# Kernel optimization log

Hardware: AMD Instinct MI355X
Metric: run time of the kernel (lower is better)

The kernel has to match this reference:

```python
import jax, jax.numpy as jnp
import numpy as np

CLAMP = 60.0
EPS = 1e-4

def _make_weights(N, alpha_logits, delta_logits, beta_logits):
    alpha = jax.nn.sigmoid(alpha_logits)   # [C,H]
    delta = jax.nn.sigmoid(delta_logits)
    beta = jax.nn.sigmoid(beta_logits)
    A = alpha * beta                        # [C,H]
    r = jnp.clip(1.0 - alpha * delta, EPS, 1.0 - EPS)
    t = jnp.arange(N, dtype=jnp.float32)[:, None, None]   # [N,1,1]
    logr = jnp.clip(jnp.log(r) * t, -CLAMP, CLAMP)        # [N,C,H]
    return A, jnp.exp(logr), jnp.exp(-logr)

def _ema_fwd(x, A, eta, r_pos, r_neg):
    # x: [B,N,C] -> y: [B,N,C]
    z = A * x[..., None] * r_neg            # [B,N,C,H]
    h = jnp.cumsum(z, axis=1) * r_pos       # [B,N,C,H]
    return jnp.sum(eta * h, axis=-1)        # [B,N,C]

def reference(x, alpha_logits, delta_logits, beta_logits, eta, proj_w, proj_b):
    B, N, C = x.shape
    A, r_pos, r_neg = _make_weights(N, alpha_logits, delta_logits, beta_logits)
    xf = x.astype(jnp.float32)
    y_fwd = _ema_fwd(xf, A, eta, r_pos, r_neg)
    y_bwd = _ema_fwd(xf[:, ::-1], A, eta, r_pos, r_neg)[:, ::-1]
    z = jnp.concatenate([y_fwd, y_bwd], axis=-1).astype(x.dtype)  # [B,N,2C]
    return z @ proj_w.T + proj_b            # [B,N,C]

def setup_inputs():
    key = jax.random.key(0)
    ks = jax.random.split(key, 7)
    B, N, C, H = 8, 4096, 512, 4
    return {
        "x": jax.random.normal(ks[0], (B, N, C), dtype=jnp.float32),
        "alpha_logits": jax.random.normal(ks[1], (C, H), dtype=jnp.float32),
        "delta_logits": jax.random.normal(ks[2], (C, H), dtype=jnp.float32),
        "beta_logits": jax.random.normal(ks[3], (C, H), dtype=jnp.float32),
        "eta": jax.random.normal(ks[4], (C, H), dtype=jnp.float32) * 0.02,
        "proj_w": jax.random.normal(ks[5], (C, 2 * C), dtype=jnp.float32) / np.sqrt(2.0 * C),
        "proj_b": jax.random.normal(ks[6], (C,), dtype=jnp.float32) * 0.01,
    }
```

## Files before the change

kernel.cpp:

```cpp
#include <hip/hip_runtime.h>
#include <hip/hip_bf16.h>

#define B_ 8
#define N_ 4096
#define C_ 512
#define H_ 4
#define EPS_ 1e-4f
#define E60P 1.14200739e26f
#define E60M 8.7565108e-27f

typedef __attribute__((ext_vector_type(8))) short short8;
typedef __attribute__((ext_vector_type(4))) float floatx4;
typedef unsigned short ushort_t;

__device__ __forceinline__ float sigmoidf_(float v) {
    return 1.0f / (1.0f + expf(-v));
}

__device__ __forceinline__ int pk_off(int t, int w, int k0, int ks, int f,
                                      int lane8, int kb) {
    return ((((t * 2 + w) * 16 + k0) * 2 + ks) * 4 + f) * 512 + lane8 * 8 + kb;
}

__global__ __launch_bounds__(256) void k_partials3(
    const float* __restrict__ x, const float* __restrict__ al,
    const float* __restrict__ dl, const float* __restrict__ bl,
    float* __restrict__ P)
{
    int bid   = blockIdx.x;
    int chunk = bid & 15;
    int ct    = (bid >> 4) & 7;
    int b     = bid >> 7;
    int lane  = threadIdx.x & 63;
    int wave  = threadIdx.x >> 6;
    int c     = ct * 64 + lane;
    int sub   = chunk * 4 + wave;
    int t0f   = sub * 64;
    int t0b   = (63 - sub) * 64;

    float aa[4], dd[4], bb[4];
    { float4 v = ((const float4*)al)[c]; aa[0]=v.x; aa[1]=v.y; aa[2]=v.z; aa[3]=v.w; }
    { float4 v = ((const float4*)dl)[c]; dd[0]=v.x; dd[1]=v.y; dd[2]=v.z; dd[3]=v.w; }
    { float4 v = ((const float4*)bl)[c]; bb[0]=v.x; bb[1]=v.y; bb[2]=v.z; bb[3]=v.w; }

    float A[H_], ri[H_], Lh[H_];
    #pragma unroll
    for (int h = 0; h < H_; ++h) {
        float alpha = sigmoidf_(aa[h]);
        float delta = sigmoidf_(dd[h]);
        float beta  = sigmoidf_(bb[h]);
        A[h] = alpha * beta;
        float r = fminf(fmaxf(1.0f - alpha * delta, EPS_), 1.0f - EPS_);
        Lh[h] = logf(r);
        ri[h] = 1.0f / r;
    }

    const float* xp = x + ((size_t)b * N_ + t0f) * C_ + c;

    float ep[H_], T[H_];
    #pragma unroll
    for (int h = 0; h < H_; ++h) {
        ep[h] = expf(fminf(-Lh[h] * (float)t0f, 60.0f));
        T[h]  = 0.0f;
    }
    #pragma unroll 8
    for (int i = 0; i < 64; ++i) {
        float xv = xp[(size_t)i * C_];
        #pragma unroll
        for (int h = 0; h < H_; ++h) {
            T[h]  = fmaf(A[h] * xv, ep[h], T[h]);
            ep[h] = fminf(ep[h] * ri[h], E60P);
        }
    }
    {
        float* pp = P + ((size_t)b * 64 + sub) * (H_ * C_) + c;
        #pragma unroll
        for (int h = 0; h < H_; ++h) pp[h * C_] = T[h];
    }

    #pragma unroll
    for (int h = 0; h < H_; ++h) {
        ep[h] = expf(fminf(-Lh[h] * (float)t0b, 60.0f));
        T[h]  = 0.0f;
    }
    #pragma unroll 8
    for (int j = 0; j < 64; ++j) {
        float xv = xp[(size_t)(63 - j) * C_];
        #pragma unroll
        for (int h = 0; h < H_; ++h) {
            T[h]  = fmaf(A[h] * xv, ep[h], T[h]);
            ep[h] = fminf(ep[h] * ri[h], E60P);
        }
    }
    {
        float* pp = P + ((size_t)(8 + b) * 64 + (63 - sub)) * (H_ * C_) + c;
        #pragma unroll
        for (int h = 0; h < H_; ++h) pp[h * C_] = T[h];
    }
}

__global__ __launch_bounds__(256) void k_scan(float* __restrict__ P)
{
    int bid = blockIdx.x;
    int ct  = bid & 7;
    int b   = (bid >> 3) & 7;
    int dir = bid >> 6;
    int cl  = threadIdx.x & 63;
    int h   = threadIdx.x >> 6;
    int c   = ct * 64 + cl;

    float run = 0.0f;
    float* base = P + ((size_t)(dir * 8 + b) * 64) * (H_ * C_) + h * C_ + c;
    for (int s = 0; s < 64; ++s) {
        float v = base[s * (H_ * C_)];
        base[s * (H_ * C_)] = run;
        run += v;
    }
}

__global__ __launch_bounds__(256) void k_apply3(
    const float* __restrict__ x, const float* __restrict__ al,
    const float* __restrict__ dl, const float* __restrict__ bl,
    const float* __restrict__ eta, const float* __restrict__ P,
    ushort_t* __restrict__ Zp)
{
    int bid   = blockIdx.x;
    int chunk = bid & 15;
    int ct    = (bid >> 4) & 7;
    int b     = bid >> 7;
    int lane  = threadIdx.x & 63;
    int wave  = threadIdx.x >> 6;
    int c     = ct * 64 + lane;
    int sub   = chunk * 4 + wave;
    int t0f   = sub * 64;
    int t0b   = (63 - sub) * 64;

    int ksv = lane >> 5, qv = (lane >> 3) & 3, kbv = lane & 7;
    int k0f = ct;
    int k0b = 8 + ct;

    float aa[4], dd[4], bb[4], ee[4];
    { float4 v = ((const float4*)al )[c]; aa[0]=v.x; aa[1]=v.y; aa[2]=v.z; aa[3]=v.w; }
    { float4 v = ((const float4*)dl )[c]; dd[0]=v.x; dd[1]=v.y; dd[2]=v.z; dd[3]=v.w; }
    { float4 v = ((const float4*)bl )[c]; bb[0]=v.x; bb[1]=v.y; bb[2]=v.z; bb[3]=v.w; }
    { float4 v = ((const float4*)eta)[c]; ee[0]=v.x; ee[1]=v.y; ee[2]=v.z; ee[3]=v.w; }

    float A[H_], rr[H_], ri[H_], Lh[H_];
    #pragma unroll
    for (int h = 0; h < H_; ++h) {
        float alpha = sigmoidf_(aa[h]);
        float delta = sigmoidf_(dd[h]);
        float beta  = sigmoidf_(bb[h]);
        A[h] = alpha * beta;
        float r = fminf(fmaxf(1.0f - alpha * delta, EPS_), 1.0f - EPS_);
        Lh[h] = logf(r);
        rr[h] = r;
        ri[h] = 1.0f / r;
    }

    const float* xp = x + ((size_t)b * N_ + t0f) * C_ + c;

    {
        const float* cp = P + ((size_t)b * 64 + sub) * (H_ * C_) + c;
        float ep[H_], em[H_], S[H_];
        #pragma unroll
        for (int h = 0; h < H_; ++h) {
            ep[h] = expf(fminf(-Lh[h] * (float)t0f, 60.0f));
            em[h] = expf(fmaxf( Lh[h] * (float)t0f, -60.0f));
            S[h]  = cp[h * C_];
        }
        #pragma unroll 4
        for (int i = 0; i < 64; ++i) {
            int n  = t0f + i;
            float xv = xp[(size_t)i * C_];
            float y = 0.0f;
            #pragma unroll
            for (int h = 0; h < H_; ++h) {
                S[h]  = fmaf(A[h] * xv, ep[h], S[h]);
                ep[h] = fminf(ep[h] * ri[h], E60P);
                y     = fmaf(ee[h], em[h] * S[h], y);
                em[h] = fmaxf(em[h] * rr[h], E60M);
            }
            int rm = n & 127, mt = b * 32 + (n >> 7);
            int off = pk_off(mt, rm >> 6, k0f, ksv, (rm >> 4) & 3,
                             qv * 16 + (rm & 15), kbv);
            __hip_bfloat16 yb = __float2bfloat16(y);
            Zp[off] = *(ushort_t*)&yb;
        }
    }

    {
        const float* cp = P + ((size_t)(8 + b) * 64 + (63 - sub)) * (H_ * C_) + c;
        float ep[H_], em[H_], S[H_];
        #pragma unroll
        for (int h = 0; h < H_; ++h) {
            ep[h] = expf(fminf(-Lh[h] * (float)t0b, 60.0f));
            em[h] = expf(fmaxf( Lh[h] * (float)t0b, -60.0f));
            S[h]  = cp[h * C_];
        }
        #pragma unroll 4
        for (int j = 0; j < 64; ++j) {
            int n  = t0f + 63 - j;
            float xv = xp[(size_t)(63 - j) * C_];
            float y = 0.0f;
            #pragma unroll
            for (int h = 0; h < H_; ++h) {
                S[h]  = fmaf(A[h] * xv, ep[h], S[h]);
                ep[h] = fminf(ep[h] * ri[h], E60P);
                y     = fmaf(ee[h], em[h] * S[h], y);
                em[h] = fmaxf(em[h] * rr[h], E60M);
            }
            int rm = n & 127, mt = b * 32 + (n >> 7);
            int off = pk_off(mt, rm >> 6, k0b, ksv, (rm >> 4) & 3,
                             qv * 16 + (rm & 15), kbv);
            __hip_bfloat16 yb = __float2bfloat16(y);
            Zp[off] = *(ushort_t*)&yb;
        }
    }
}

__global__ __launch_bounds__(256) void k_cvtw2(const float* __restrict__ w,
                                               ushort_t* __restrict__ Wp)
{
    int i = blockIdx.x * 256 + threadIdx.x;
    int n = i >> 10, k = i & 1023;
    int nt = n >> 7, rn = n & 127;
    int k0 = k >> 6, kk = k & 63;
    int off = pk_off(nt, rn >> 6, k0, kk >> 5, (rn >> 4) & 3,
                     ((kk >> 3) & 3) * 16 + (rn & 15), kk & 7);
    __hip_bfloat16 vb = __float2bfloat16(w[i]);
    Wp[off] = *(ushort_t*)&vb;
}

__global__ __launch_bounds__(256, 2) void k_gemm2(
    const ushort_t* __restrict__ Zp, const ushort_t* __restrict__ Wp,
    const float* __restrict__ bias, float* __restrict__ out)
{
    __shared__ __align__(16) float stg[32 * 132];

    int tid  = threadIdx.x;
    int lane = tid & 63, wave = tid >> 6;
    int wm   = wave & 1, wn = wave >> 1;
    int fr   = lane & 15, quad = lane >> 4;

    int lin = blockIdx.x;
    int nt  = lin & 3, mt = lin >> 2;
    int m0  = mt * 128, n0 = nt * 128;

    const ushort_t* Ab = Zp + ((size_t)(mt * 2 + wm) * 16) * 4096 + lane * 8;
    const ushort_t* Bb = Wp + ((size_t)(nt * 2 + wn) * 16) * 4096 + lane * 8;

    floatx4 acc[4][4];
    #pragma unroll
    for (int mf = 0; mf < 4; ++mf)
        #pragma unroll
        for (int nf = 0; nf < 4; ++nf)
            acc[mf][nf] = (floatx4){0.f, 0.f, 0.f, 0.f};

    #pragma unroll
    for (int k0 = 0; k0 < 16; ++k0) {
        short8 af[2][4], bf[2][4];
        #pragma unroll
        for (int ks = 0; ks < 2; ++ks)
            #pragma unroll
            for (int f = 0; f < 4; ++f) {
                af[ks][f] = *(const short8*)(Ab + k0 * 4096 + (ks * 4 + f) * 512);
                bf[ks][f] = *(const short8*)(Bb + k0 * 4096 + (ks * 4 + f) * 512);
            }
        #pragma unroll
        for (int ks = 0; ks < 2; ++ks)
            #pragma unroll
            for (int mf = 0; mf < 4; ++mf)
                #pragma unroll
                for (int nf = 0; nf < 4; ++nf)
                    acc[mf][nf] = __builtin_amdgcn_mfma_f32_16x16x32_bf16(
                        af[ks][mf], bf[ks][nf], acc[mf][nf], 0, 0, 0);
    }

    int rrow = tid >> 3;
    int seg  = tid & 7;
    int gcol = n0 + seg * 16;

    #pragma unroll
    for (int ch = 0; ch < 4; ++ch) {
        if ((wave & 1) == (ch >> 1)) {
            int ml = (ch & 1) * 2;
            #pragma unroll
            for (int mi = 0; mi < 2; ++mi) {
                #pragma unroll
                for (int nf = 0; nf < 4; ++nf) {
                    int col = wn * 64 + nf * 16 + fr;
                    #pragma unroll
                    for (int rg = 0; rg < 4; ++rg) {
                        int row = mi * 16 + quad * 4 + rg;
                        stg[row * 132 + col] = acc[ml + mi][nf][rg];
                    }
                }
            }
        }
        __syncthreads();
        {
            int gm = m0 + ch * 32 + rrow;
            const float* s = &stg[rrow * 132 + seg * 16];
            #pragma unroll
            for (int k = 0; k < 4; ++k) {
                float4 v  = *(const float4*)&s[k * 4];
                float4 bv = *(const float4*)&bias[gcol + k * 4];
                v.x += bv.x; v.y += bv.y; v.z += bv.z; v.w += bv.w;
                *(float4*)&out[(size_t)gm * 512 + gcol + k * 4] = v;
            }
        }
        __syncthreads();
    }
}

extern "C" void kernel_launch(void* const* d_in, const int* in_sizes, int n_in,
                              void* d_out, int out_size, void* d_ws, size_t ws_size,
                              hipStream_t stream)
{
    const float* x  = (const float*)d_in[0];
    const float* al = (const float*)d_in[1];
    const float* dl = (const float*)d_in[2];
    const float* bl = (const float*)d_in[3];
    const float* et = (const float*)d_in[4];
    const float* pw = (const float*)d_in[5];
    const float* pb = (const float*)d_in[6];
    float* out = (float*)d_out;

    ushort_t* Zp = (ushort_t*)d_ws;
    float*    P  = (float*)((char*)d_ws + 67108864);
    ushort_t* Wp = (ushort_t*)((char*)d_ws + 75497472);

    hipLaunchKernelGGL(k_cvtw2,     dim3(2048), dim3(256), 0, stream, pw, Wp);
    hipLaunchKernelGGL(k_partials3, dim3(1024), dim3(256), 0, stream, x, al, dl, bl, P);
    hipLaunchKernelGGL(k_scan,      dim3(128),  dim3(256), 0, stream, P);
    hipLaunchKernelGGL(k_apply3,    dim3(1024), dim3(256), 0, stream, x, al, dl, bl, et, P, Zp);
    hipLaunchKernelGGL(k_gemm2,     dim3(1024), dim3(256), 0, stream, Zp, Wp, pb, out);
}
```

Before: 237.4 us.

## Vectorize EMA scans with packed float2, prefetch x, simplify Zp offsets, remap GEMM blocks

The partials and apply kernels now hold the four decay heads as two float2 vectors so the compiler can emit packed FP32 math, and they load the next 8 timesteps of x while the current 8 are computed. The apply kernel precomputes a base packed-layout offset per thread and adds a cheap per-step term, replacing the full pk_off index calculation. The GEMM block index mapping is changed so consecutive blocks share M tiles across N tiles, aiming at better L2 reuse. The prefetch buffers raise register pressure, and the mixed changes make attribution hard.

```diff
diff --git a/kernel.cpp b/kernel.cpp
--- a/kernel.cpp
+++ b/kernel.cpp
@@ -11,6 +11,7 @@
 
 typedef __attribute__((ext_vector_type(8))) short short8;
 typedef __attribute__((ext_vector_type(4))) float floatx4;
+typedef __attribute__((ext_vector_type(2))) float floatx2;
 typedef unsigned short ushort_t;
 
 __device__ __forceinline__ float sigmoidf_(float v) {
@@ -54,48 +55,85 @@
         Lh[h] = logf(r);
         ri[h] = 1.0f / r;
     }
+    const floatx2 E2P = {E60P, E60P};
+    floatx2 A2[2]  = {{A[0],  A[1]},  {A[2],  A[3]}};
+    floatx2 ri2[2] = {{ri[0], ri[1]}, {ri[2], ri[3]}};
 
     const float* xp = x + ((size_t)b * N_ + t0f) * C_ + c;
 
-    float ep[H_], T[H_];
-    #pragma unroll
-    for (int h = 0; h < H_; ++h) {
-        ep[h] = expf(fminf(-Lh[h] * (float)t0f, 60.0f));
-        T[h]  = 0.0f;
-    }
-    #pragma unroll 8
-    for (int i = 0; i < 64; ++i) {
-        float xv = xp[(size_t)i * C_];
-        #pragma unroll
-        for (int h = 0; h < H_; ++h) {
-            T[h]  = fmaf(A[h] * xv, ep[h], T[h]);
-            ep[h] = fminf(ep[h] * ri[h], E60P);
-        }
+    floatx2 ep2[2], T2[2];
+    #pragma unroll
+    for (int p = 0; p < 2; ++p) {
+        ep2[p] = (floatx2){expf(fminf(-Lh[2*p]   * (float)t0f, 60.0f)),
+                           expf(fminf(-Lh[2*p+1] * (float)t0f, 60.0f))};
+        T2[p]  = (floatx2){0.f, 0.f};
     }
     {
+        float cur[8];
+        #pragma unroll
+        for (int j = 0; j < 8; ++j) cur[j] = xp[(size_t)j * C_];
+        #pragma unroll 1
+        for (int g = 0; g < 8; ++g) {
+            float nxt[8];
+            if (g < 7) {
+                #pragma unroll
+                for (int j = 0; j < 8; ++j)
+                    nxt[j] = xp[(size_t)(g * 8 + 8 + j) * C_];
+            }
+            #pragma unroll
+            for (int j = 0; j < 8; ++j) {
+                floatx2 xv2 = {cur[j], cur[j]};
+                #pragma unroll
+                for (int p = 0; p < 2; ++p) {
+                    T2[p] += (A2[p] * xv2) * ep2[p];
+                    ep2[p] = __builtin_elementwise_min(ep2[p] * ri2[p], E2P);
+                }
+            }
+            if (g < 7) {
+                #pragma unroll
+                for (int j = 0; j < 8; ++j) cur[j] = nxt[j];
+            }
+        }
         float* pp = P + ((size_t)b * 64 + sub) * (H_ * C_) + c;
-        #pragma unroll
-        for (int h = 0; h < H_; ++h) pp[h * C_] = T[h];
-    }
-
-    #pragma unroll
-    for (int h = 0; h < H_; ++h) {
-        ep[h] = expf(fminf(-Lh[h] * (float)t0b, 60.0f));
-        T[h]  = 0.0f;
-    }
-    #pragma unroll 8
-    for (int j = 0; j < 64; ++j) {
-        float xv = xp[(size_t)(63 - j) * C_];
-        #pragma unroll
-        for (int h = 0; h < H_; ++h) {
-            T[h]  = fmaf(A[h] * xv, ep[h], T[h]);
-            ep[h] = fminf(ep[h] * ri[h], E60P);
-        }
+        pp[0]      = T2[0].x;  pp[C_]     = T2[0].y;
+        pp[2 * C_] = T2[1].x;  pp[3 * C_] = T2[1].y;
+    }
+
+    #pragma unroll
+    for (int p = 0; p < 2; ++p) {
+        ep2[p] = (floatx2){expf(fminf(-Lh[2*p]   * (float)t0b, 60.0f)),
+                           expf(fminf(-Lh[2*p+1] * (float)t0b, 60.0f))};
+        T2[p]  = (floatx2){0.f, 0.f};
     }
     {
+        float cur[8];
+        #pragma unroll
+        for (int j = 0; j < 8; ++j) cur[j] = xp[(size_t)(63 - j) * C_];
+        #pragma unroll 1
+        for (int g = 0; g < 8; ++g) {
+            float nxt[8];
+            if (g < 7) {
+                #pragma unroll
+                for (int j = 0; j < 8; ++j)
+                    nxt[j] = xp[(size_t)(63 - (g * 8 + 8 + j)) * C_];
+            }
+            #pragma unroll
+            for (int j = 0; j < 8; ++j) {
+                floatx2 xv2 = {cur[j], cur[j]};
+                #pragma unroll
+                for (int p = 0; p < 2; ++p) {
+                    T2[p] += (A2[p] * xv2) * ep2[p];
+                    ep2[p] = __builtin_elementwise_min(ep2[p] * ri2[p], E2P);
+                }
+            }
+            if (g < 7) {
+                #pragma unroll
+                for (int j = 0; j < 8; ++j) cur[j] = nxt[j];
+            }
+        }
         float* pp = P + ((size_t)(8 + b) * 64 + (63 - sub)) * (H_ * C_) + c;
-        #pragma unroll
-        for (int h = 0; h < H_; ++h) pp[h * C_] = T[h];
+        pp[0]      = T2[0].x;  pp[C_]     = T2[0].y;
+        pp[2 * C_] = T2[1].x;  pp[3 * C_] = T2[1].y;
     }
 }
 
@@ -136,8 +174,10 @@
     int t0b   = (63 - sub) * 64;
 
     int ksv = lane >> 5, qv = (lane >> 3) & 3, kbv = lane & 7;
-    int k0f = ct;
-    int k0b = 8 + ct;
+    int mt  = b * 32 + (t0f >> 7);
+    int wq  = (t0f >> 6) & 1;
+    int offcF = pk_off(mt, wq, ct,     ksv, 0, qv * 16, kbv);
+    int offcB = pk_off(mt, wq, 8 + ct, ksv, 0, qv * 16, kbv);
 
     float aa[4], dd[4], bb[4], ee[4];
     { float4 v = ((const float4*)al )[c]; aa[0]=v.x; aa[1]=v.y; aa[2]=v.z; aa[3]=v.w; }
@@ -157,64 +197,102 @@
         rr[h] = r;
         ri[h] = 1.0f / r;
     }
+    const floatx2 E2P = {E60P, E60P};
+    const floatx2 E2M = {E60M, E60M};
+    floatx2 A2[2]  = {{A[0],  A[1]},  {A[2],  A[3]}};
+    floatx2 ri2[2] = {{ri[0], ri[1]}, {ri[2], ri[3]}};
+    floatx2 rr2[2] = {{rr[0], rr[1]}, {rr[2], rr[3]}};
+    floatx2 ee2[2] = {{ee[0], ee[1]}, {ee[2], ee[3]}};
 
     const float* xp = x + ((size_t)b * N_ + t0f) * C_ + c;
 
     {
         const float* cp = P + ((size_t)b * 64 + sub) * (H_ * C_) + c;
-        float ep[H_], em[H_], S[H_];
-        #pragma unroll
-        for (int h = 0; h < H_; ++h) {
-            ep[h] = expf(fminf(-Lh[h] * (float)t0f, 60.0f));
-            em[h] = expf(fmaxf( Lh[h] * (float)t0f, -60.0f));
-            S[h]  = cp[h * C_];
-        }
-        #pragma unroll 4
-        for (int i = 0; i < 64; ++i) {
-            int n  = t0f + i;
-            float xv = xp[(size_t)i * C_];
-            float y = 0.0f;
-            #pragma unroll
-            for (int h = 0; h < H_; ++h) {
-                S[h]  = fmaf(A[h] * xv, ep[h], S[h]);
-                ep[h] = fminf(ep[h] * ri[h], E60P);
-                y     = fmaf(ee[h], em[h] * S[h], y);
-                em[h] = fmaxf(em[h] * rr[h], E60M);
-            }
-            int rm = n & 127, mt = b * 32 + (n >> 7);
-            int off = pk_off(mt, rm >> 6, k0f, ksv, (rm >> 4) & 3,
-                             qv * 16 + (rm & 15), kbv);
-            __hip_bfloat16 yb = __float2bfloat16(y);
-            Zp[off] = *(ushort_t*)&yb;
+        floatx2 ep2[2], em2[2], S2[2];
+        #pragma unroll
+        for (int p = 0; p < 2; ++p) {
+            ep2[p] = (floatx2){expf(fminf(-Lh[2*p]   * (float)t0f, 60.0f)),
+                               expf(fminf(-Lh[2*p+1] * (float)t0f, 60.0f))};
+            em2[p] = (floatx2){expf(fmaxf( Lh[2*p]   * (float)t0f, -60.0f)),
+                               expf(fmaxf( Lh[2*p+1] * (float)t0f, -60.0f))};
+            S2[p]  = (floatx2){cp[(2*p) * C_], cp[(2*p+1) * C_]};
+        }
+        float cur[8];
+        #pragma unroll
+        for (int j = 0; j < 8; ++j) cur[j] = xp[(size_t)j * C_];
+        #pragma unroll 1
+        for (int g = 0; g < 8; ++g) {
+            float nxt[8];
+            if (g < 7) {
+                #pragma unroll
+                for (int j = 0; j < 8; ++j)
+                    nxt[j] = xp[(size_t)(g * 8 + 8 + j) * C_];
+            }
+            #pragma unroll
+            for (int j = 0; j < 8; ++j) {
+                int i = g * 8 + j;
+                floatx2 xv2 = {cur[j], cur[j]};
+                floatx2 acc = {0.f, 0.f};
+                #pragma unroll
+                for (int p = 0; p < 2; ++p) {
+                    S2[p] += (A2[p] * xv2) * ep2[p];
+                    ep2[p] = __builtin_elementwise_min(ep2[p] * ri2[p], E2P);
+                    acc   += ee2[p] * (em2[p] * S2[p]);
+                    em2[p] = __builtin_elementwise_max(em2[p] * rr2[p], E2M);
+                }
+                float y = acc.x + acc.y;
+                __hip_bfloat16 yb = __float2bfloat16(y);
+                Zp[offcF + (i >> 4) * 512 + (i & 15) * 8] = *(ushort_t*)&yb;
+            }
+            if (g < 7) {
+                #pragma unroll
+                for (int j = 0; j < 8; ++j) cur[j] = nxt[j];
+            }
         }
     }
 
     {
         const float* cp = P + ((size_t)(8 + b) * 64 + (63 - sub)) * (H_ * C_) + c;
-        float ep[H_], em[H_], S[H_];
-        #pragma unroll
-        for (int h = 0; h < H_; ++h) {
-            ep[h] = expf(fminf(-Lh[h] * (float)t0b, 60.0f));
-            em[h] = expf(fmaxf( Lh[h] * (float)t0b, -60.0f));
-            S[h]  = cp[h * C_];
-        }
-        #pragma unroll 4
-        for (int j = 0; j < 64; ++j) {
-            int n  = t0f + 63 - j;
-            float xv = xp[(size_t)(63 - j) * C_];
-            float y = 0.0f;
-            #pragma unroll
-            for (int h = 0; h < H_; ++h) {
-                S[h]  = fmaf(A[h] * xv, ep[h], S[h]);
-                ep[h] = fminf(ep[h] * ri[h], E60P);
-                y     = fmaf(ee[h], em[h] * S[h], y);
-                em[h] = fmaxf(em[h] * rr[h], E60M);
-            }
-            int rm = n & 127, mt = b * 32 + (n >> 7);
-            int off = pk_off(mt, rm >> 6, k0b, ksv, (rm >> 4) & 3,
-                             qv * 16 + (rm & 15), kbv);
-            __hip_bfloat16 yb = __float2bfloat16(y);
-            Zp[off] = *(ushort_t*)&yb;
+        floatx2 ep2[2], em2[2], S2[2];
+        #pragma unroll
+        for (int p = 0; p < 2; ++p) {
+            ep2[p] = (floatx2){expf(fminf(-Lh[2*p]   * (float)t0b, 60.0f)),
+                               expf(fminf(-Lh[2*p+1] * (float)t0b, 60.0f))};
+            em2[p] = (floatx2){expf(fmaxf( Lh[2*p]   * (float)t0b, -60.0f)),
+                               expf(fmaxf( Lh[2*p+1] * (float)t0b, -60.0f))};
+            S2[p]  = (floatx2){cp[(2*p) * C_], cp[(2*p+1) * C_]};
+        }
+        float cur[8];
+        #pragma unroll
+        for (int j = 0; j < 8; ++j) cur[j] = xp[(size_t)(63 - j) * C_];
+        #pragma unroll 1
+        for (int g = 0; g < 8; ++g) {
+            float nxt[8];
+            if (g < 7) {
+                #pragma unroll
+                for (int j = 0; j < 8; ++j)
+                    nxt[j] = xp[(size_t)(63 - (g * 8 + 8 + j)) * C_];
+            }
+            #pragma unroll
+            for (int j = 0; j < 8; ++j) {
+                int i = 63 - (g * 8 + j);
+                floatx2 xv2 = {cur[j], cur[j]};
+                floatx2 acc = {0.f, 0.f};
+                #pragma unroll
+                for (int p = 0; p < 2; ++p) {
+                    S2[p] += (A2[p] * xv2) * ep2[p];
+                    ep2[p] = __builtin_elementwise_min(ep2[p] * ri2[p], E2P);
+                    acc   += ee2[p] * (em2[p] * S2[p]);
+                    em2[p] = __builtin_elementwise_max(em2[p] * rr2[p], E2M);
+                }
+                float y = acc.x + acc.y;
+                __hip_bfloat16 yb = __float2bfloat16(y);
+                Zp[offcB + (i >> 4) * 512 + (i & 15) * 8] = *(ushort_t*)&yb;
+            }
+            if (g < 7) {
+                #pragma unroll
+                for (int j = 0; j < 8; ++j) cur[j] = nxt[j];
+            }
         }
     }
 }
@@ -243,8 +321,9 @@
     int wm   = wave & 1, wn = wave >> 1;
     int fr   = lane & 15, quad = lane >> 4;
 
-    int lin = blockIdx.x;
-    int nt  = lin & 3, mt = lin >> 2;
+    int bid = blockIdx.x;
+    int mt  = ((bid >> 5) << 3) | (bid & 7);
+    int nt  = (bid >> 3) & 3;
     int m0  = mt * 128, n0 = nt * 128;
 
     const ushort_t* Ab = Zp + ((size_t)(mt * 2 + wm) * 16) * 4096 + lane * 8;
```

Measured after the change: 229.0 us. 3.5% less time.
